# Kernel tuning notes

Hardware: AMD Instinct MI355X
Metric: run time of the kernel (lower is better)

## Reference

```python
import jax, jax.numpy as jnp
import numpy as np

# Model dims
B, S, H, NH = 2, 2048, 1024, 8
HD = H // NH            # head_dim = 128
T = S * NH              # MoE input tokens per batch = 16384
E, K, F = 8, 2, 512     # experts, top_k, expert FFN dim (4*head_dim)


def setup_inputs() -> dict:
    key = jax.random.key(0)
    ks = jax.random.split(key, 9)
    s = 0.02  # init scale
    return {
        "x": jax.random.normal(ks[0], (B, S, H), jnp.float32),
        "W_mh": jax.random.normal(ks[1], (H, H), jnp.float32) * s,
        "b_mh": jnp.zeros((H,), jnp.float32),
        "W_merge": jax.random.normal(ks[2], (H, H), jnp.float32) * s,
        "b_merge": jnp.zeros((H,), jnp.float32),
        "W_router": jax.random.normal(ks[3], (HD, E), jnp.float32) * s,
        "W1": jax.random.normal(ks[4], (E, HD, F), jnp.float32) * s,
        "b1": jnp.zeros((E, F), jnp.float32),
        "W2": jax.random.normal(ks[5], (E, F, HD), jnp.float32) * s,
        "b2": jnp.zeros((E, HD), jnp.float32),
    }


def reference(x, W_mh, b_mh, W_merge, b_merge, W_router, W1, b1, W2, b2):
    # multi-head projection then split heads into the token axis
    h = x @ W_mh + b_mh                       # [B, S, H]
    h = h.reshape(B, T, HD)                   # [B, T, HD]

    # nested VectorizedMoE: top-k token-choice routing over head_dim tokens
    logits = h @ W_router                     # [B, T, E]
    probs = jax.nn.softmax(logits, axis=-1)
    topv, topi = jax.lax.top_k(probs, K)      # [B, T, K]
    topv = topv / jnp.sum(topv, axis=-1, keepdims=True)  # renormalize top-k gates
    # scatter top-k gates into dense [B, T, E] combine weights
    gates = jnp.sum(jax.nn.one_hot(topi, E, dtype=h.dtype) * topv[..., None], axis=-2)

    # vectorized expert FFNs (all experts, combined with sparse gates)
    a = jax.nn.gelu(jnp.einsum('btd,edf->btef', h, W1) + b1)   # [B, T, E, F]
    y = jnp.einsum('btef,efd->bted', a, W2) + b2               # [B, T, E, HD]
    moe_out = jnp.einsum('bte,bted->btd', gates, y)            # [B, T, HD]

    # merge heads back and final projection
    out = moe_out.reshape(B, S, H) @ W_merge + b_merge         # [B, S, H]
    return out
```

## Files before the change

kernel.cpp:

```cpp
#include <hip/hip_runtime.h>


typedef __attribute__((ext_vector_type(8))) short bf16x8;
typedef __attribute__((ext_vector_type(4))) float f32x4;
typedef __attribute__((ext_vector_type(16))) float f32x16;
typedef __attribute__((ext_vector_type(4))) unsigned short u16x4;

constexpr int NSLOT = 66560;
constexpr int NTILE_MAX = 520;
#define CTRL_CNT 0
#define CTRL_CUR 8

__device__ __forceinline__ unsigned short f2bf(float x) {
  unsigned int u = __float_as_uint(x);
  return (unsigned short)((u + 0x7FFFu + ((u >> 16) & 1u)) >> 16);
}
__device__ __forceinline__ float bf2f(unsigned short u) {
  return __uint_as_float(((unsigned int)u) << 16);
}
__device__ __forceinline__ void gload_lds16(const void* g, void* l) {
  __builtin_amdgcn_global_load_lds(
      (const __attribute__((address_space(1))) unsigned int*)g,
      (__attribute__((address_space(3))) unsigned int*)l, 16, 0, 0);
}

__global__ __launch_bounds__(256) void prep_all(
    const float* __restrict__ Wmh, unsigned short* __restrict__ Wmh_t,
    const float* __restrict__ Wmg, unsigned short* __restrict__ Wmg_t,
    const float* __restrict__ W1, const float* __restrict__ W2,
    unsigned short* __restrict__ W1F, unsigned short* __restrict__ W2F,
    const float* __restrict__ bmh, const float* __restrict__ Wr,
    float* __restrict__ Wc, int* __restrict__ ctrl) {
  __shared__ float smem[2048];
  const int bid = blockIdx.x, tid = threadIdx.x;
  if (bid < 2048) {
    if (bid == 0 && tid < 16) ctrl[tid] = 0;
    const float* src = (bid < 1024) ? Wmh : Wmg;
    unsigned short* dst = (bid < 1024) ? Wmh_t : Wmg_t;
    const int bb = bid & 1023;
    const int c0 = (bb & 31) * 32, r0 = (bb >> 5) * 32;
    const int tx = tid & 31, ty = tid >> 5;
    float (*tile)[33] = (float(*)[33])smem;
    for (int i = ty; i < 32; i += 8)
      tile[i][tx] = src[(size_t)(r0 + i) * 1024 + c0 + tx];
    __syncthreads();
    for (int i = ty; i < 32; i += 8)
      dst[(size_t)(c0 + i) * 1024 + r0 + tx] = f2bf(tile[tx][i]);
  } else if (bid < 2560) {
    const int jid = (bid - 2048) * 4 + (tid >> 6);
    const int l = tid & 63;
    const int is2 = jid >= 1024;
    const int bj = is2 ? jid - 1024 : jid;
    const float* src;
    int C;
    if (!is2) {
      int kk = bj & 7, ft = (bj >> 3) & 15, e = bj >> 7;
      src = W1 + (size_t)e * 65536 + (size_t)(kk * 16) * 512 + ft * 32;
      C = 512;
    } else {
      int sht = bj & 7, ft = (bj >> 3) & 15, e = bj >> 7;
      src = W2 + (size_t)e * 65536 + (size_t)(ft * 32 + (sht >> 2) * 16) * 128 + (sht & 3) * 32;
      C = 128;
    }
    float* tile = smem + (tid >> 6) * 512;
#pragma unroll
    for (int r = 0; r < 8; ++r) {
      int i = l + 64 * r;
      tile[(i >> 5) * 32 + (i & 31)] = src[(size_t)(i >> 5) * C + (i & 31)];
    }
    __syncthreads();
    int l31 = l & 31, lh = l >> 5;
    bf16x8 v;
#pragma unroll
    for (int j = 0; j < 8; ++j) v[j] = (short)f2bf(tile[(lh * 8 + j) * 32 + l31]);
    unsigned short* dst = is2 ? W2F : W1F;
    *(bf16x8*)(dst + ((size_t)bj * 64 + l) * 8) = v;
  } else {
    const int r = (bid - 2560) * 4 + (tid >> 6);
    if (r > 1024) return;
    const int l = tid & 63;
    const float* src = (r < 1024) ? (Wmh + (size_t)r * 1024) : bmh;
    int nh = l >> 3, e = l & 7;
    float acc = 0.f;
    for (int d = 0; d < 128; ++d) acc = fmaf(src[nh * 128 + d], Wr[d * 8 + e], acc);
    Wc[(size_t)r * 64 + l] = acc;
  }
}

__global__ __launch_bounds__(256) void router_partial(
    const float* __restrict__ x, const float* __restrict__ Wc,
    float* __restrict__ part, unsigned short* __restrict__ x_bf,
    int* __restrict__ perm, float* __restrict__ gateb) {
  const int tid = threadIdx.x;
  const int kc = blockIdx.x, rb = blockIdx.y;
  int gi = (rb * 8 + kc) * 256 + tid;
  if (gi < NSLOT) { perm[gi] = 0; gateb[gi] = 0.f; }

  __shared__ float xs[32][128];
  __shared__ float wcs[128][64];
  const int r0 = rb * 32, k0 = kc * 128;

  for (int f = tid; f < 1024; f += 256) {
    int row = f >> 5, j4 = (f & 31) * 4;
    float4 v = *(const float4*)&x[(size_t)(r0 + row) * 1024 + k0 + j4];
    *(float4*)&xs[row][j4] = v;
    u16x4 o;
    o.x = f2bf(v.x); o.y = f2bf(v.y); o.z = f2bf(v.z); o.w = f2bf(v.w);
    *(u16x4*)&x_bf[(size_t)(r0 + row) * 1024 + k0 + j4] = o;
  }
  {
    const float4* src = (const float4*)(Wc + (size_t)k0 * 64);
    float4* dst = (float4*)&wcs[0][0];
    for (int f = tid; f < 2048; f += 256) dst[f] = src[f];
  }
  __syncthreads();

  const int col = tid & 63, rg = tid >> 6;
  float a[8] = {0.f, 0.f, 0.f, 0.f, 0.f, 0.f, 0.f, 0.f};
  for (int k4 = 0; k4 < 32; ++k4) {
    float4 xv[8];
#pragma unroll
    for (int i = 0; i < 8; ++i)
      xv[i] = *(const float4*)&xs[rg * 8 + i][k4 * 4];
#pragma unroll
    for (int u = 0; u < 4; ++u) {
      float wv = wcs[k4 * 4 + u][col];
#pragma unroll
      for (int i = 0; i < 8; ++i)
        a[i] = fmaf((&xv[i].x)[u], wv, a[i]);
    }
  }
#pragma unroll
  for (int i = 0; i < 8; ++i)
    part[(size_t)kc * 262144 + (size_t)(r0 + rg * 8 + i) * 64 + col] = a[i];
}

__global__ __launch_bounds__(256) void router_reduce(
    const float* __restrict__ part, const float* __restrict__ Wc,
    int* __restrict__ tok_e, float* __restrict__ tok_g,
    int* __restrict__ ctrl) {
  __shared__ float lg[32][64];
  __shared__ int lcnt[8];
  const int tid = threadIdx.x;
  if (tid < 8) lcnt[tid] = 0;
  const int r0 = blockIdx.x * 32;
  const int col = tid & 63, rg = tid >> 6;
#pragma unroll
  for (int i = 0; i < 8; ++i) {
    size_t base = (size_t)(r0 + rg * 8 + i) * 64 + col;
    float s = Wc[65536 + col];
#pragma unroll
    for (int kc = 0; kc < 8; ++kc) s += part[(size_t)kc * 262144 + base];
    lg[rg * 8 + i][col] = s;
  }
  __syncthreads();
  {
    int row = tid >> 3, nh = tid & 7;
    float l[8];
#pragma unroll
    for (int e = 0; e < 8; ++e) l[e] = lg[row][nh * 8 + e];
    int i1 = 0; float v1 = l[0];
#pragma unroll
    for (int e = 1; e < 8; ++e) if (l[e] > v1) { v1 = l[e]; i1 = e; }
    int i2 = -1; float v2 = -1e30f;
#pragma unroll
    for (int e = 0; e < 8; ++e) if (e != i1 && l[e] > v2) { v2 = l[e]; i2 = e; }
    float g1 = 1.f / (1.f + __expf(v2 - v1));
    float g2 = 1.f - g1;
    size_t t = (size_t)(r0 + row) * 8 + nh;
    tok_e[t * 2] = i1; tok_e[t * 2 + 1] = i2;
    tok_g[t * 2] = g1; tok_g[t * 2 + 1] = g2;
    atomicAdd(&lcnt[i1], 1);
    atomicAdd(&lcnt[i2], 1);
  }
  __syncthreads();
  if (tid < 8 && lcnt[tid])
    atomicAdd(&ctrl[CTRL_CNT + tid], lcnt[tid]);
}

__global__ __launch_bounds__(256) void assign_kernel(
    const int* __restrict__ tok_e, const float* __restrict__ tok_g,
    int* __restrict__ ctrl, int* __restrict__ perm,
    float* __restrict__ gateb, int* __restrict__ tok_slot) {
  __shared__ int lcnt[8], lbase[8];
  if (threadIdx.x < 8) lcnt[threadIdx.x] = 0;
  __syncthreads();
  int t = blockIdx.x * 256 + threadIdx.x;
  int e0 = tok_e[t * 2], e1 = tok_e[t * 2 + 1];
  int p0 = atomicAdd(&lcnt[e0], 1);
  int p1 = atomicAdd(&lcnt[e1], 1);
  __syncthreads();
  if (threadIdx.x < 8)
    lbase[threadIdx.x] = atomicAdd(&ctrl[CTRL_CUR + threadIdx.x], lcnt[threadIdx.x]);
  __syncthreads();
  int off0 = 0, off1 = 0, acc = 0;
#pragma unroll
  for (int i = 0; i < 8; ++i) {
    int cnt = ctrl[CTRL_CNT + i];
    if (i == e0) off0 = acc;
    if (i == e1) off1 = acc;
    acc += (cnt + 127) & ~127;
  }
  int s0 = off0 + lbase[e0] + p0;
  int s1 = off1 + lbase[e1] + p1;
  perm[s0] = t; perm[s1] = t;
  gateb[s0] = tok_g[t * 2]; gateb[s1] = tok_g[t * 2 + 1];
  tok_slot[t * 2] = s0; tok_slot[t * 2 + 1] = s1;
}

template <int OUT_BF16, int A_GATHER>
__global__ __launch_bounds__(512, 4) void gemm_bt(
    const unsigned short* __restrict__ A, const unsigned short* __restrict__ Bt,
    const float* __restrict__ bias, void* __restrict__ Cout,
    int M, int N, int K,
    const unsigned short* __restrict__ ybuf, const int* __restrict__ tok_slot) {
  __shared__ __align__(16) unsigned short As[2][128 * 64];
  __shared__ __align__(16) unsigned short Bs[2][128 * 64];
  const int tid = threadIdx.x, lane = tid & 63, w = tid >> 6;
  const int wr = w >> 1, wc = w & 1;
  const int m0 = blockIdx.x * 128, n0 = blockIdx.y * 128;
  const int l15 = lane & 15, lhi = lane >> 4;

  f32x4 acc[2][4];
#pragma unroll
  for (int n = 0; n < 4; ++n) {
    float bv = bias[n0 + wc * 64 + n * 16 + l15];
#pragma unroll
    for (int m = 0; m < 2; ++m) acc[m][n] = (f32x4){bv, bv, bv, bv};
  }

  const int rowi = tid >> 3;
  const int segi = (tid & 7) * 8;
  const int NT = K >> 6;

  auto stage = [&](int buf, int kt) {
    const int k0 = kt * 64;
    if constexpr (A_GATHER) {
#pragma unroll
      for (int r = 0; r < 2; ++r) {
        int arow = m0 + r * 64 + rowi;
        int k = k0 + segi;
        int tok = arow * 8 + (k >> 7);
        int hd = k & 127;
        int s0 = tok_slot[tok * 2], s1 = tok_slot[tok * 2 + 1];
        bf16x8 va = *(const bf16x8*)(ybuf + (size_t)s0 * 128 + hd);
        bf16x8 vb = *(const bf16x8*)(ybuf + (size_t)s1 * 128 + hd);
        bf16x8 vs;
#pragma unroll
        for (int j = 0; j < 8; ++j)
          vs[j] = (short)f2bf(bf2f((unsigned short)va[j]) + bf2f((unsigned short)vb[j]));
        *(bf16x8*)&As[buf][r * 4096 + tid * 8] = vs;
      }
    } else {
#pragma unroll
      for (int r = 0; r < 2; ++r)
        gload_lds16(A + (size_t)(m0 + r * 64 + rowi) * K + k0 + segi,
                    &As[buf][r * 4096 + w * 512]);
    }
#pragma unroll
    for (int r = 0; r < 2; ++r)
      gload_lds16(Bt + (size_t)(n0 + r * 64 + rowi) * K + k0 + segi,
                  &Bs[buf][r * 4096 + w * 512]);
  };

  stage(0, 0);
  asm volatile("s_waitcnt vmcnt(0)" ::: "memory");
  __syncthreads();
  int cur = 0;
  for (int t = 0; t < NT; ++t) {
    if (t + 1 < NT) stage(cur ^ 1, t + 1);
#pragma unroll
    for (int ks = 0; ks < 64; ks += 32) {
      bf16x8 af[2], bb[4];
#pragma unroll
      for (int m = 0; m < 2; ++m)
        af[m] = *(const bf16x8*)&As[cur][(wr * 32 + m * 16 + l15) * 64 + ks + lhi * 8];
#pragma unroll
      for (int n = 0; n < 4; ++n)
        bb[n] = *(const bf16x8*)&Bs[cur][(wc * 64 + n * 16 + l15) * 64 + ks + lhi * 8];
#pragma unroll
      for (int m = 0; m < 2; ++m)
#pragma unroll
        for (int n = 0; n < 4; ++n)
          acc[m][n] = __builtin_amdgcn_mfma_f32_16x16x32_bf16(af[m], bb[n], acc[m][n], 0, 0, 0);
    }
    asm volatile("s_waitcnt vmcnt(0)" ::: "memory");
    __syncthreads();
    cur ^= 1;
  }
#pragma unroll
  for (int m = 0; m < 2; ++m) {
#pragma unroll
    for (int n = 0; n < 4; ++n) {
      int col = n0 + wc * 64 + n * 16 + l15;
#pragma unroll
      for (int j = 0; j < 4; ++j) {
        int row = m0 + wr * 32 + m * 16 + lhi * 4 + j;
        if (OUT_BF16)
          ((unsigned short*)Cout)[(size_t)row * N + col] = f2bf(acc[m][n][j]);
        else
          ((float*)Cout)[(size_t)row * N + col] = acc[m][n][j];
      }
    }
  }
}

__global__ __launch_bounds__(256, 2) void ffn_sparse_v3(
    const unsigned short* __restrict__ hbf,
    const int* __restrict__ ctrl,
    const int* __restrict__ perm,
    const float* __restrict__ gateb,
    const unsigned short* __restrict__ W1F,
    const float* __restrict__ b1,
    const unsigned short* __restrict__ W2F,
    const float* __restrict__ b2,
    unsigned short* __restrict__ ybuf) {
  int e = -1;
  {
    int accT = 0;
#pragma unroll
    for (int i = 0; i < 8; ++i) {
      int tiles = (ctrl[CTRL_CNT + i] + 127) >> 7;
      if (e < 0 && (int)blockIdx.x < accT + tiles) e = i;
      accT += tiles;
    }
  }
  if (e < 0) return;
  __shared__ unsigned short W1c[2][4096];
  __shared__ unsigned short W2c[2][4096];
  __shared__ float b1_s[512];
  __shared__ float b2_s[128];
  const int tid = threadIdx.x, l = tid & 63, w = tid >> 6;
  const int l31 = l & 31, lh = l >> 5;
  const int slot = blockIdx.x * 128 + w * 32 + l31;
  const int prow = perm[slot];
  const float gate = gateb[slot];

  bf16x8 hreg[8];
  const unsigned short* hsrc = hbf + (size_t)prow * 128 + lh * 8;
#pragma unroll
  for (int kk = 0; kk < 8; ++kk)
    hreg[kk] = *(const bf16x8*)(hsrc + kk * 16);

  if (tid < 128) ((float4*)b1_s)[tid] = ((const float4*)(b1 + e * 512))[tid];
  if (tid < 32)  ((float4*)b2_s)[tid] = ((const float4*)(b2 + e * 128))[tid];

  const unsigned short* W1e = W1F + (size_t)e * 65536;
  const unsigned short* W2e = W2F + (size_t)e * 65536;
  auto stage = [&](int buf, int ft) {
#pragma unroll
    for (int r = 0; r < 2; ++r) {
      gload_lds16(W1e + (size_t)ft * 4096 + (size_t)(r * 256 + tid) * 8,
                  &W1c[buf][r * 2048 + w * 512]);
      gload_lds16(W2e + (size_t)ft * 4096 + (size_t)(r * 256 + tid) * 8,
                  &W2c[buf][r * 2048 + w * 512]);
    }
  };

  stage(0, 0);
  asm volatile("s_waitcnt vmcnt(0)" ::: "memory");
  __syncthreads();

  f32x16 yacc[4] = {};
  int cur = 0;
  for (int ft = 0; ft < 16; ++ft) {
    if (ft < 15) stage(cur ^ 1, ft + 1);
    const float4* b14 = (const float4*)b1_s;
    float4 q0 = b14[ft * 8 + lh];
    float4 q1 = b14[ft * 8 + lh + 2];
    float4 q2 = b14[ft * 8 + lh + 4];
    float4 q3 = b14[ft * 8 + lh + 6];
    f32x16 aacc = {q0.x, q0.y, q0.z, q0.w, q1.x, q1.y, q1.z, q1.w,
                   q2.x, q2.y, q2.z, q2.w, q3.x, q3.y, q3.z, q3.w};
#pragma unroll
    for (int kk = 0; kk < 8; ++kk) {
      bf16x8 a1 = *(const bf16x8*)&W1c[cur][(kk * 64 + l) * 8];
      aacc = __builtin_amdgcn_mfma_f32_32x32x16_bf16(a1, hreg[kk], aacc, 0, 0, 0);
    }
    float ge[16];
#pragma unroll
    for (int r = 0; r < 16; ++r) {
      float v = aacc[r];
      float s2 = v * v;
      float q = fmaf(0.1029432f, s2, 2.3022078f);
      float E = exp2f(v * q);
      float rc = __builtin_amdgcn_rcpf(E + 1.f);
      ge[r] = fmaf(-v, rc, v) * gate;
    }
    unsigned pk[8];
#pragma unroll
    for (int p = 0; p < 8; ++p) {
      unsigned r;
      asm("v_cvt_pk_bf16_f32 %0, %1, %2" : "=v"(r) : "v"(ge[2 * p]), "v"(ge[2 * p + 1]));
      pk[p] = r;
    }
    asm volatile("v_permlane32_swap_b32 %0, %1" : "+v"(pk[0]), "+v"(pk[2]));
    asm volatile("v_permlane32_swap_b32 %0, %1" : "+v"(pk[1]), "+v"(pk[3]));
    asm volatile("v_permlane32_swap_b32 %0, %1" : "+v"(pk[4]), "+v"(pk[6]));
    asm volatile("v_permlane32_swap_b32 %0, %1" : "+v"(pk[5]), "+v"(pk[7]));
    typedef __attribute__((ext_vector_type(4))) unsigned u32x4;
    u32x4 f0 = {pk[0], pk[1], pk[2], pk[3]};
    u32x4 f1 = {pk[4], pk[5], pk[6], pk[7]};
    bf16x8 act0 = __builtin_bit_cast(bf16x8, f0);
    bf16x8 act1 = __builtin_bit_cast(bf16x8, f1);
#pragma unroll
    for (int ht = 0; ht < 4; ++ht) {
      bf16x8 a20 = *(const bf16x8*)&W2c[cur][(ht * 64 + l) * 8];
      yacc[ht] = __builtin_amdgcn_mfma_f32_32x32x16_bf16(a20, act0, yacc[ht], 0, 0, 0);
      bf16x8 a21 = *(const bf16x8*)&W2c[cur][((4 + ht) * 64 + l) * 8];
      yacc[ht] = __builtin_amdgcn_mfma_f32_32x32x16_bf16(a21, act1, yacc[ht], 0, 0, 0);
    }
    asm volatile("s_waitcnt vmcnt(0)" ::: "memory");
    __syncthreads();
    cur ^= 1;
  }
#pragma unroll
  for (int ht = 0; ht < 4; ++ht) {
#pragma unroll
    for (int rp = 0; rp < 8; ++rp) {
      int fr = ((2 * rp) & 3) + 8 * (rp >> 1) + 4 * lh;
      int hd = ht * 32 + fr;
      float2 bb2 = *(const float2*)&b2_s[hd];
      float v0 = fmaf(gate, bb2.x, yacc[ht][2 * rp]);
      float v1 = fmaf(gate, bb2.y, yacc[ht][2 * rp + 1]);
      unsigned pw;
      asm("v_cvt_pk_bf16_f32 %0, %1, %2" : "=v"(pw) : "v"(v0), "v"(v1));
      *(unsigned*)(ybuf + (size_t)slot * 128 + hd) = pw;
    }
  }
}

extern "C" void kernel_launch(void* const* d_in, const int* in_sizes, int n_in,
                              void* d_out, int out_size, void* d_ws, size_t ws_size,
                              hipStream_t stream) {
  const float* x       = (const float*)d_in[0];
  const float* W_mh    = (const float*)d_in[1];
  const float* b_mh    = (const float*)d_in[2];
  const float* W_merge = (const float*)d_in[3];
  const float* b_merge = (const float*)d_in[4];
  const float* W_rout  = (const float*)d_in[5];
  const float* W1      = (const float*)d_in[6];
  const float* b1      = (const float*)d_in[7];
  const float* W2      = (const float*)d_in[8];
  const float* b2      = (const float*)d_in[9];
  float* out = (float*)d_out;

  char* ws = (char*)d_ws;
  size_t off = 0;
  auto alloc = [&](size_t bytes) {
    void* p = ws + off;
    off = (off + bytes + 255) & ~(size_t)255;
    return p;
  };
  unsigned short* x_bf  = (unsigned short*)alloc((size_t)4096 * 1024 * 2);
  unsigned short* Wmh_t = (unsigned short*)alloc((size_t)1024 * 1024 * 2);
  unsigned short* Wmg_t = (unsigned short*)alloc((size_t)1024 * 1024 * 2);
  unsigned short* W1F   = (unsigned short*)alloc((size_t)8 * 512 * 128 * 2);
  unsigned short* W2F   = (unsigned short*)alloc((size_t)8 * 512 * 128 * 2);
  unsigned short* h_bf  = (unsigned short*)alloc((size_t)4096 * 1024 * 2);
  unsigned short* ybuf  = (unsigned short*)alloc((size_t)NSLOT * 128 * 2);
  float* Wc             = (float*)alloc((size_t)1025 * 64 * 4);
  float* part           = (float*)alloc((size_t)8 * 4096 * 64 * 4);
  int*   ctrl           = (int*)alloc(4096);
  int*   tok_e          = (int*)alloc((size_t)32768 * 2 * 4);
  float* tok_g          = (float*)alloc((size_t)32768 * 2 * 4);
  int*   tok_slot       = (int*)alloc((size_t)32768 * 2 * 4);
  int*   perm           = (int*)alloc((size_t)NSLOT * 4);
  float* gateb          = (float*)alloc((size_t)NSLOT * 4);

  prep_all<<<2817, 256, 0, stream>>>(W_mh, Wmh_t, W_merge, Wmg_t,
                                     W1, W2, W1F, W2F, b_mh, W_rout, Wc, ctrl);
  router_partial<<<dim3(8, 128), 256, 0, stream>>>(x, Wc, part, x_bf, perm, gateb);
  router_reduce<<<128, 256, 0, stream>>>(part, Wc, tok_e, tok_g, ctrl);
  assign_kernel<<<128, 256, 0, stream>>>(tok_e, tok_g, ctrl, perm, gateb, tok_slot);
  gemm_bt<1, 0><<<dim3(32, 8), 512, 0, stream>>>(x_bf, Wmh_t, b_mh, (void*)h_bf,
                                                 4096, 1024, 1024, nullptr, nullptr);
  ffn_sparse_v3<<<NTILE_MAX, 256, 0, stream>>>(h_bf, ctrl, perm, gateb, W1F, b1, W2F, b2, ybuf);
  gemm_bt<0, 1><<<dim3(32, 8), 512, 0, stream>>>(nullptr, Wmg_t, b_merge, (void*)out,
                                                 4096, 1024, 1024, ybuf, tok_slot);
}
```

Measured before the change: 139.3 us.

## Split expert FFN hidden dimension across two blocks with partial output buffers

The sparse expert FFN kernel now launches two blocks per token tile, each covering half of the 512-wide hidden dimension, and writes its partial second-layer output to a separate buffer (bias added only by the first half). The merge GEMM gathers and sums the four partial results per token while staging A. This doubles FFN parallelism to fill more CUs, but each block reloads the h rows and the merge kernel reads twice as much y data, with an extra bf16 rounding on the partials.

```diff
diff --git a/kernel.cpp b/kernel.cpp
--- a/kernel.cpp
+++ b/kernel.cpp
@@ -213,7 +213,9 @@
     const unsigned short* __restrict__ A, const unsigned short* __restrict__ Bt,
     const float* __restrict__ bias, void* __restrict__ Cout,
     int M, int N, int K,
-    const unsigned short* __restrict__ ybuf, const int* __restrict__ tok_slot) {
+    const unsigned short* __restrict__ ybufA,
+    const unsigned short* __restrict__ ybufB,
+    const int* __restrict__ tok_slot) {
   __shared__ __align__(16) unsigned short As[2][128 * 64];
   __shared__ __align__(16) unsigned short Bs[2][128 * 64];
   const int tid = threadIdx.x, lane = tid & 63, w = tid >> 6;
@@ -243,12 +245,17 @@
         int tok = arow * 8 + (k >> 7);
         int hd = k & 127;
         int s0 = tok_slot[tok * 2], s1 = tok_slot[tok * 2 + 1];
-        bf16x8 va = *(const bf16x8*)(ybuf + (size_t)s0 * 128 + hd);
-        bf16x8 vb = *(const bf16x8*)(ybuf + (size_t)s1 * 128 + hd);
+        bf16x8 va0 = *(const bf16x8*)(ybufA + (size_t)s0 * 128 + hd);
+        bf16x8 vb0 = *(const bf16x8*)(ybufB + (size_t)s0 * 128 + hd);
+        bf16x8 va1 = *(const bf16x8*)(ybufA + (size_t)s1 * 128 + hd);
+        bf16x8 vb1 = *(const bf16x8*)(ybufB + (size_t)s1 * 128 + hd);
         bf16x8 vs;
 #pragma unroll
-        for (int j = 0; j < 8; ++j)
-          vs[j] = (short)f2bf(bf2f((unsigned short)va[j]) + bf2f((unsigned short)vb[j]));
+        for (int j = 0; j < 8; ++j) {
+          float p = bf2f((unsigned short)va0[j]) + bf2f((unsigned short)vb0[j]);
+          float q = bf2f((unsigned short)va1[j]) + bf2f((unsigned short)vb1[j]);
+          vs[j] = (short)f2bf(p + q);
+        }
         *(bf16x8*)&As[buf][r * 4096 + tid * 8] = vs;
       }
     } else {
@@ -305,7 +312,7 @@
   }
 }
 
-__global__ __launch_bounds__(256, 2) void ffn_sparse_v3(
+__global__ __launch_bounds__(256, 2) void ffn_sparse_v9(
     const unsigned short* __restrict__ hbf,
     const int* __restrict__ ctrl,
     const int* __restrict__ perm,
@@ -314,14 +321,16 @@
     const float* __restrict__ b1,
     const unsigned short* __restrict__ W2F,
     const float* __restrict__ b2,
-    unsigned short* __restrict__ ybuf) {
+    unsigned short* __restrict__ ybufA,
+    unsigned short* __restrict__ ybufB) {
+  const int tile = blockIdx.x >> 1, fh = blockIdx.x & 1;
   int e = -1;
   {
     int accT = 0;
 #pragma unroll
     for (int i = 0; i < 8; ++i) {
       int tiles = (ctrl[CTRL_CNT + i] + 127) >> 7;
-      if (e < 0 && (int)blockIdx.x < accT + tiles) e = i;
+      if (e < 0 && tile < accT + tiles) e = i;
       accT += tiles;
     }
   }
@@ -332,7 +341,7 @@
   __shared__ float b2_s[128];
   const int tid = threadIdx.x, l = tid & 63, w = tid >> 6;
   const int l31 = l & 31, lh = l >> 5;
-  const int slot = blockIdx.x * 128 + w * 32 + l31;
+  const int slot = tile * 128 + w * 32 + l31;
   const int prow = perm[slot];
   const float gate = gateb[slot];
 
@@ -357,14 +366,16 @@
     }
   };
 
-  stage(0, 0);
+  const int ftbase = fh * 8;
+  stage(0, ftbase);
   asm volatile("s_waitcnt vmcnt(0)" ::: "memory");
   __syncthreads();
 
   f32x16 yacc[4] = {};
   int cur = 0;
-  for (int ft = 0; ft < 16; ++ft) {
-    if (ft < 15) stage(cur ^ 1, ft + 1);
+  for (int it = 0; it < 8; ++it) {
+    const int ft = ftbase + it;
+    if (it < 7) stage(cur ^ 1, ft + 1);
     const float4* b14 = (const float4*)b1_s;
     float4 q0 = b14[ft * 8 + lh];
     float4 q1 = b14[ft * 8 + lh + 2];
@@ -414,18 +425,23 @@
     __syncthreads();
     cur ^= 1;
   }
+  unsigned short* yout = fh ? ybufB : ybufA;
 #pragma unroll
   for (int ht = 0; ht < 4; ++ht) {
 #pragma unroll
     for (int rp = 0; rp < 8; ++rp) {
       int fr = ((2 * rp) & 3) + 8 * (rp >> 1) + 4 * lh;
       int hd = ht * 32 + fr;
-      float2 bb2 = *(const float2*)&b2_s[hd];
-      float v0 = fmaf(gate, bb2.x, yacc[ht][2 * rp]);
-      float v1 = fmaf(gate, bb2.y, yacc[ht][2 * rp + 1]);
+      float v0 = yacc[ht][2 * rp];
+      float v1 = yacc[ht][2 * rp + 1];
+      if (fh == 0) {
+        float2 bb2 = *(const float2*)&b2_s[hd];
+        v0 = fmaf(gate, bb2.x, v0);
+        v1 = fmaf(gate, bb2.y, v1);
+      }
       unsigned pw;
       asm("v_cvt_pk_bf16_f32 %0, %1, %2" : "=v"(pw) : "v"(v0), "v"(v1));
-      *(unsigned*)(ybuf + (size_t)slot * 128 + hd) = pw;
+      *(unsigned*)(yout + (size_t)slot * 128 + hd) = pw;
     }
   }
 }
@@ -458,7 +474,8 @@
   unsigned short* W1F   = (unsigned short*)alloc((size_t)8 * 512 * 128 * 2);
   unsigned short* W2F   = (unsigned short*)alloc((size_t)8 * 512 * 128 * 2);
   unsigned short* h_bf  = (unsigned short*)alloc((size_t)4096 * 1024 * 2);
-  unsigned short* ybuf  = (unsigned short*)alloc((size_t)NSLOT * 128 * 2);
+  unsigned short* ybufA = (unsigned short*)alloc((size_t)NSLOT * 128 * 2);
+  unsigned short* ybufB = (unsigned short*)alloc((size_t)NSLOT * 128 * 2);
   float* Wc             = (float*)alloc((size_t)1025 * 64 * 4);
   float* part           = (float*)alloc((size_t)8 * 4096 * 64 * 4);
   int*   ctrl           = (int*)alloc(4096);
@@ -474,8 +491,9 @@
   router_reduce<<<128, 256, 0, stream>>>(part, Wc, tok_e, tok_g, ctrl);
   assign_kernel<<<128, 256, 0, stream>>>(tok_e, tok_g, ctrl, perm, gateb, tok_slot);
   gemm_bt<1, 0><<<dim3(32, 8), 512, 0, stream>>>(x_bf, Wmh_t, b_mh, (void*)h_bf,
-                                                 4096, 1024, 1024, nullptr, nullptr);
-  ffn_sparse_v3<<<NTILE_MAX, 256, 0, stream>>>(h_bf, ctrl, perm, gateb, W1F, b1, W2F, b2, ybuf);
+                                                 4096, 1024, 1024, nullptr, nullptr, nullptr);
+  ffn_sparse_v9<<<NTILE_MAX * 2, 256, 0, stream>>>(h_bf, ctrl, perm, gateb,
+                                                   W1F, b1, W2F, b2, ybufA, ybufB);
   gemm_bt<0, 1><<<dim3(32, 8), 512, 0, stream>>>(nullptr, Wmg_t, b_merge, (void*)out,
-                                                 4096, 1024, 1024, ybuf, tok_slot);
-}
+                                                 4096, 1024, 1024, ybufA, ybufB, tok_slot);
+}
```

New measurement: 154.6 us. +11.0%, slower.
